# Optimization experiments

Measured on AMD Instinct MI355X. Metric: run time of the kernel, lower is better.

The kernel has to match this reference:

```python
import jax, jax.numpy as jnp
import numpy as np

B, S, D, H = 8192, 45, 64, 8
HD = D // H          # head_dim = 8
FF = 4 * D           # FFN inner dim = 256


def _layernorm(x, g, b, eps=1e-5):
    m = x.mean(-1, keepdims=True)
    v = ((x - m) ** 2).mean(-1, keepdims=True)
    return (x - m) * jax.lax.rsqrt(v + eps) * g + b


def setup_inputs() -> dict:
    key = jax.random.key(0)
    ks = jax.random.split(key, 8)
    s = 1.0 / np.sqrt(D)
    sf = 1.0 / np.sqrt(FF)
    return {
        "x": jax.random.normal(ks[0], (B, S, D), jnp.float32),
        "Wq": jax.random.normal(ks[1], (D, D), jnp.float32) * s,
        "bq": jnp.zeros((D,), jnp.float32),
        "Wk": jax.random.normal(ks[2], (D, D), jnp.float32) * s,
        "bk": jnp.zeros((D,), jnp.float32),
        "Wv": jax.random.normal(ks[3], (D, D), jnp.float32) * s,
        "bv": jnp.zeros((D,), jnp.float32),
        "Wo": jax.random.normal(ks[4], (D, D), jnp.float32) * s,
        "bo": jnp.zeros((D,), jnp.float32),
        "ln1_g": jnp.ones((D,), jnp.float32),
        "ln1_b": jnp.zeros((D,), jnp.float32),
        "W1": jax.random.normal(ks[5], (D, FF), jnp.float32) * s,
        "b1": jnp.zeros((FF,), jnp.float32),
        "W2": jax.random.normal(ks[6], (FF, D), jnp.float32) * sf,
        "b2": jnp.zeros((D,), jnp.float32),
        "ln2_g": jnp.ones((D,), jnp.float32),
        "ln2_b": jnp.zeros((D,), jnp.float32),
    }


def reference(x, Wq, bq, Wk, bk, Wv, bv, Wo, bo, ln1_g, ln1_b, W1, b1, W2, b2, ln2_g, ln2_b):
    b, s, d = x.shape
    # sinusoidal positional encoding (PositionalEncoding(hidden_dim, max_len=45))
    pos = jnp.arange(s, dtype=jnp.float32)[:, None]
    div = jnp.exp(-jnp.log(jnp.float32(10000.0)) * jnp.arange(0, d, 2, dtype=jnp.float32) / d)
    ang = pos * div                              # [S, D/2]
    pe = jnp.zeros((s, d), x.dtype).at[:, 0::2].set(jnp.sin(ang)).at[:, 1::2].set(jnp.cos(ang))
    h = x + pe                                   # [B, S, D]
    residual = h
    # torch.nn.MultiheadAttention, batch_first=True, 8 heads, head_dim 8
    q = (h @ Wq + bq).reshape(b, s, H, HD).transpose(0, 2, 1, 3)  # [B,H,S,HD]
    k = (h @ Wk + bk).reshape(b, s, H, HD).transpose(0, 2, 1, 3)
    v = (h @ Wv + bv).reshape(b, s, H, HD).transpose(0, 2, 1, 3)
    scores = jnp.einsum('bhqd,bhkd->bhqk', q, k) / jnp.sqrt(jnp.float32(HD))
    attn = jax.nn.softmax(scores, axis=-1)
    o = jnp.einsum('bhqk,bhkd->bhqd', attn, v).transpose(0, 2, 1, 3).reshape(b, s, d)
    o = o @ Wo + bo
    # norm(out + alpha * residual), alpha = 1
    h2 = _layernorm(o + residual, ln1_g, ln1_b)
    # FFN: Linear -> ReLU -> Linear, residual + LayerNorm (standard transformer FFN)
    f = jax.nn.relu(h2 @ W1 + b1) @ W2 + b2
    return _layernorm(h2 + f, ln2_g, ln2_b)
```

## Files before the change

kernel.cpp:

```cpp
#include <hip/hip_runtime.h>
#include <math.h>

#define NB 8192
#define S_ 45
#define D_ 64
#define FF_ 256
#define LDH 68
#define HBS 72
#define VTS 56
#define FBH 136

typedef __attribute__((ext_vector_type(4))) float f32x4;
typedef __attribute__((ext_vector_type(8))) short s16x8;
typedef __attribute__((ext_vector_type(4))) short s16x4;

#define WS_QKV 11520
#define WS_WO  36096
#define WS_W1  44288
#define WS_W2  77056

__device__ inline short f2bf(float f) {
    union { float f; unsigned u; } c; c.f = f;
    unsigned u = c.u;
    return (short)((u + 0x7FFFu + ((u >> 16) & 1u)) >> 16);
}
__device__ inline float bf2f(short s) {
    union { unsigned u; float f; } c;
    c.u = ((unsigned)(unsigned short)s) << 16;
    return c.f;
}

__global__ void prep_kernel(const float* __restrict__ Wq, const float* __restrict__ Wk,
                            const float* __restrict__ Wv, const float* __restrict__ Wo,
                            const float* __restrict__ W1, const float* __restrict__ W2,
                            void* __restrict__ ws) {
    float* pe   = (float*)ws;
    short* wqkv = (short*)((char*)ws + WS_QKV);
    short* wo   = (short*)((char*)ws + WS_WO);
    short* w1   = (short*)((char*)ws + WS_W1);
    short* w2   = (short*)((char*)ws + WS_W2);
    int i = blockIdx.x * 256 + threadIdx.x;
    if (i < S_ * D_) {
        int s = i / D_, d = i % D_;
        float div = expf(-logf(10000.0f) * (float)(d & ~1) / (float)D_);
        float ang = (float)s * div;
        pe[i] = (d & 1) ? cosf(ang) : sinf(ang);
    }
    if (i < 12288) {
        int n = i >> 6, k = i & 63;
        const float* W = (n < 64) ? Wq : (n < 128 ? Wk : Wv);
        wqkv[i] = f2bf(W[k * 64 + (n & 63)]);
    }
    if (i < 4096) {
        int n = i >> 6, k = i & 63;
        wo[i] = f2bf(Wo[k * 64 + n]);
    }
    if (i < 16384) {
        int n = i >> 6, k = i & 63;
        w1[i] = f2bf(W1[k * FF_ + n]);
        int n2 = i >> 8, k2 = i & 255;
        w2[i] = f2bf(W2[k2 * 64 + n2]);
    }
}

__launch_bounds__(512, 1)
__global__ void encoder_kernel(
    const float* __restrict__ x,
    const float* __restrict__ bq, const float* __restrict__ bk,
    const float* __restrict__ bv, const float* __restrict__ bo,
    const float* __restrict__ ln1g, const float* __restrict__ ln1b,
    const float* __restrict__ b1, const float* __restrict__ b2,
    const float* __restrict__ ln2g, const float* __restrict__ ln2b,
    const void* __restrict__ ws,
    float* __restrict__ out)
{
    const float* pe    = (const float*)ws;
    const short* wqkvT = (const short*)((const char*)ws + WS_QKV);
    const short* woT   = (const short*)((const char*)ws + WS_WO);
    const short* w1T   = (const short*)((const char*)ws + WS_W1);
    const short* w2T   = (const short*)((const char*)ws + WS_W2);

    __shared__ __align__(16) char pool[28800];
    short* hb = (short*)pool;
    short* qb = (short*)(pool + 6912);
    short* kb = (short*)(pool + 13824);
    short* vT = (short*)(pool + 20736);
    short* ob = qb;
    float* t1 = (float*)(pool + 13824);
    short* fb = (short*)(pool + 13824);
    float* t2 = (float*)(pool + 13824);

    const int t = threadIdx.x;
    const int b = blockIdx.x;
    const int w = t >> 6, l = t & 63;
    const int lr = l & 15, lg = l >> 4;
    const s16x8 zero8 = {0, 0, 0, 0, 0, 0, 0, 0};

    {
        const float4* x4 = (const float4*)(x + (size_t)b * (S_ * D_));
        const float4* p4 = (const float4*)pe;
        for (int i = t; i < S_ * D_ / 4; i += 512) {
            int r = i >> 4, c4 = (i & 15) << 2;
            float4 a = x4[i], p = p4[i];
            s16x4 hv16 = { f2bf(a.x + p.x), f2bf(a.y + p.y),
                           f2bf(a.z + p.z), f2bf(a.w + p.w) };
            *(s16x4*)&hb[r * HBS + c4] = hv16;
        }
        for (int i = t; i < 3 * HBS; i += 512) hb[45 * HBS + i] = 0;
    }
    __syncthreads();

    {
        const float SC2 = 0.35355339059327373f * 1.44269504088896340f;
        for (int id = w; id < 36; id += 8) {
            const int m0 = (id % 3) << 4, n0 = (id / 3) << 4;
            f32x4 acc = {0.f, 0.f, 0.f, 0.f};
            #pragma unroll
            for (int k0 = 0; k0 < 64; k0 += 32) {
                s16x8 af = *(const s16x8*)&hb[(m0 + lr) * HBS + k0 + lg * 8];
                s16x8 bf = *(const s16x8*)&wqkvT[(n0 + lr) * 64 + k0 + lg * 8];
                acc = __builtin_amdgcn_mfma_f32_16x16x32_bf16(af, bf, acc, 0, 0, 0);
            }
            if (n0 < 64) {
                const float bias = bq[n0 + lr];
                #pragma unroll
                for (int r = 0; r < 4; ++r)
                    qb[(m0 + lg * 4 + r) * HBS + n0 + lr] = f2bf((acc[r] + bias) * SC2);
            } else if (n0 < 128) {
                const int cc = n0 - 64 + lr;
                const float bias = bk[cc];
                #pragma unroll
                for (int r = 0; r < 4; ++r)
                    kb[(m0 + lg * 4 + r) * HBS + cc] = f2bf(acc[r] + bias);
            } else {
                const int cc = n0 - 128 + lr;
                const float bias = bv[cc];
                s16x4 vv = { f2bf(acc[0] + bias), f2bf(acc[1] + bias),
                             f2bf(acc[2] + bias), f2bf(acc[3] + bias) };
                *(s16x4*)&vT[cc * VTS + m0 + lg * 4] = vv;
            }
        }
    }
    __syncthreads();

    {
        const int hd = w << 3;
        s16x8 pv_b0 = *(const s16x8*)&vT[(hd + lr) * VTS + lg * 8];
        s16x8 pv_b1 = (lg < 2) ? *(const s16x8*)&vT[(hd + lr) * VTS + 32 + lg * 8]
                               : zero8;
        f32x4 O[3];
        #pragma unroll
        for (int tn = 0; tn < 3; ++tn) {
            s16x8 qbf = (lg == 0) ? *(const s16x8*)&qb[(tn * 16 + lr) * HBS + hd] : zero8;
            f32x4 S[3];
            #pragma unroll
            for (int tm = 0; tm < 3; ++tm) {
                s16x8 kaf = (lg == 0) ? *(const s16x8*)&kb[(tm * 16 + lr) * HBS + hd] : zero8;
                f32x4 z = {0.f, 0.f, 0.f, 0.f};
                S[tm] = __builtin_amdgcn_mfma_f32_16x16x32_bf16(kaf, qbf, z, 0, 0, 0);
            }
            float psum = 0.f;
            #pragma unroll
            for (int tm = 0; tm < 3; ++tm) {
                #pragma unroll
                for (int r = 0; r < 4; ++r) {
                    float e = __builtin_amdgcn_exp2f(S[tm][r]);
                    if (tm == 2) e = (lg * 4 + r >= 13) ? 0.f : e;
                    S[tm][r] = e;
                    psum += e;
                }
            }
            float s = psum;
            s += __shfl_xor(s, 16);
            s += __shfl_xor(s, 32);
            float inv = 1.0f / s;
            unsigned pk0[3], pk1[3];
            #pragma unroll
            for (int tm = 0; tm < 3; ++tm) {
                float a0 = S[tm][0] * inv, a1 = S[tm][1] * inv;
                float a2 = S[tm][2] * inv, a3 = S[tm][3] * inv;
                pk0[tm] = (__float_as_uint(a0) >> 16) | (__float_as_uint(a1) & 0xFFFF0000u);
                pk1[tm] = (__float_as_uint(a2) >> 16) | (__float_as_uint(a3) & 0xFFFF0000u);
            }
            const int srcA = lr + ((lg & 1) << 5);
            const int srcB = srcA + 16;
            unsigned gA0[3], gA1[3], gB0[3], gB1[3];
            #pragma unroll
            for (int tm = 0; tm < 3; ++tm) {
                gA0[tm] = (unsigned)__shfl((int)pk0[tm], srcA);
                gA1[tm] = (unsigned)__shfl((int)pk1[tm], srcA);
                gB0[tm] = (unsigned)__shfl((int)pk0[tm], srcB);
                gB1[tm] = (unsigned)__shfl((int)pk1[tm], srcB);
            }
            const bool tm1 = (lg >> 1) != 0;
            union { unsigned u[4]; s16x8 v; } a1c, a2c;
            a1c.u[0] = tm1 ? gA0[1] : gA0[0];
            a1c.u[1] = tm1 ? gA1[1] : gA1[0];
            a1c.u[2] = tm1 ? gB0[1] : gB0[0];
            a1c.u[3] = tm1 ? gB1[1] : gB1[0];
            const bool lo = (lg < 2);
            a2c.u[0] = lo ? gA0[2] : 0u;
            a2c.u[1] = lo ? gA1[2] : 0u;
            a2c.u[2] = lo ? gB0[2] : 0u;
            a2c.u[3] = lo ? gB1[2] : 0u;
            f32x4 z = {0.f, 0.f, 0.f, 0.f};
            O[tn] = __builtin_amdgcn_mfma_f32_16x16x32_bf16(a1c.v, pv_b0, z, 0, 0, 0);
            O[tn] = __builtin_amdgcn_mfma_f32_16x16x32_bf16(a2c.v, pv_b1, O[tn], 0, 0, 0);
        }
        __syncthreads();
        if (lr < 8) {
            #pragma unroll
            for (int tn = 0; tn < 3; ++tn)
                #pragma unroll
                for (int r = 0; r < 4; ++r) {
                    int row = tn * 16 + lg * 4 + r;
                    if (row < S_) ob[row * HBS + hd + lr] = f2bf(O[tn][r]);
                }
        }
    }
    __syncthreads();

    {
        for (int id = w; id < 12; id += 8) {
            const int m0 = (id % 3) << 4, n0 = (id / 3) << 4;
            f32x4 acc = {0.f, 0.f, 0.f, 0.f};
            #pragma unroll
            for (int k0 = 0; k0 < 64; k0 += 32) {
                s16x8 af = *(const s16x8*)&ob[(m0 + lr) * HBS + k0 + lg * 8];
                s16x8 bf = *(const s16x8*)&woT[(n0 + lr) * 64 + k0 + lg * 8];
                acc = __builtin_amdgcn_mfma_f32_16x16x32_bf16(af, bf, acc, 0, 0, 0);
            }
            const int col = n0 + lr;
            const float bias = bo[col];
            #pragma unroll
            for (int r = 0; r < 4; ++r) {
                int row = m0 + lg * 4 + r;
                if (row < S_)
                    t1[row * LDH + col] = acc[r] + bias + bf2f(hb[row * HBS + col]);
            }
        }
    }
    __syncthreads();

    {
        const int wv = t >> 6, d = t & 63;
        const float g = ln1g[d], bb = ln1b[d];
        for (int i = 0; i < 6; ++i) {
            int r = wv + 8 * i;
            if (r < S_) {
                float v = t1[r * LDH + d];
                float s = v, s2 = v * v;
                #pragma unroll
                for (int off = 32; off; off >>= 1) {
                    s  += __shfl_xor(s, off);
                    s2 += __shfl_xor(s2, off);
                }
                float mean = s * (1.0f / 64.0f);
                float var  = s2 * (1.0f / 64.0f) - mean * mean;
                float nv = (v - mean) * rsqrtf(var + 1e-5f);
                hb[r * HBS + d] = f2bf(nv * g + bb);
            }
        }
    }
    __syncthreads();

    f32x4 facc0 = {0.f, 0.f, 0.f, 0.f};
    f32x4 facc1 = {0.f, 0.f, 0.f, 0.f};
    for (int hx = 0; hx < 2; ++hx) {
        for (int id = w; id < 24; id += 8) {
            const int m0 = (id % 3) << 4, nl = (id / 3) << 4;
            f32x4 acc = {0.f, 0.f, 0.f, 0.f};
            #pragma unroll
            for (int k0 = 0; k0 < 64; k0 += 32) {
                s16x8 af = *(const s16x8*)&hb[(m0 + lr) * HBS + k0 + lg * 8];
                s16x8 bf = *(const s16x8*)&w1T[(hx * 128 + nl + lr) * 64 + k0 + lg * 8];
                acc = __builtin_amdgcn_mfma_f32_16x16x32_bf16(af, bf, acc, 0, 0, 0);
            }
            const float bias = b1[hx * 128 + nl + lr];
            #pragma unroll
            for (int r = 0; r < 4; ++r) {
                int row = m0 + lg * 4 + r;
                if (row < S_)
                    fb[row * FBH + nl + lr] = f2bf(fmaxf(acc[r] + bias, 0.f));
            }
        }
        __syncthreads();
        {
            const int m0 = (w % 3) << 4, n0 = (w / 3) << 4;
            #pragma unroll
            for (int k0 = 0; k0 < 128; k0 += 32) {
                s16x8 af = *(const s16x8*)&fb[(m0 + lr) * FBH + k0 + lg * 8];
                s16x8 bf = *(const s16x8*)&w2T[(n0 + lr) * 256 + hx * 128 + k0 + lg * 8];
                facc0 = __builtin_amdgcn_mfma_f32_16x16x32_bf16(af, bf, facc0, 0, 0, 0);
            }
        }
        if (w < 4) {
            const int id = w + 8;
            const int m0 = (id % 3) << 4, n0 = (id / 3) << 4;
            #pragma unroll
            for (int k0 = 0; k0 < 128; k0 += 32) {
                s16x8 af = *(const s16x8*)&fb[(m0 + lr) * FBH + k0 + lg * 8];
                s16x8 bf = *(const s16x8*)&w2T[(n0 + lr) * 256 + hx * 128 + k0 + lg * 8];
                facc1 = __builtin_amdgcn_mfma_f32_16x16x32_bf16(af, bf, facc1, 0, 0, 0);
            }
        }
        __syncthreads();
    }
    {
        const int m0 = (w % 3) << 4, n0 = (w / 3) << 4;
        const int col = n0 + lr;
        const float bias = b2[col];
        #pragma unroll
        for (int r = 0; r < 4; ++r) {
            int row = m0 + lg * 4 + r;
            if (row < S_)
                t2[row * LDH + col] = facc0[r] + bias + bf2f(hb[row * HBS + col]);
        }
        if (w < 4) {
            const int id = w + 8;
            const int m1 = (id % 3) << 4, n1 = (id / 3) << 4;
            const int col1 = n1 + lr;
            const float bias1 = b2[col1];
            #pragma unroll
            for (int r = 0; r < 4; ++r) {
                int row = m1 + lg * 4 + r;
                if (row < S_)
                    t2[row * LDH + col1] = facc1[r] + bias1 + bf2f(hb[row * HBS + col1]);
            }
        }
    }
    __syncthreads();

    {
        const int wv = t >> 6, d = t & 63;
        const float g = ln2g[d], bb = ln2b[d];
        for (int i = 0; i < 6; ++i) {
            int r = wv + 8 * i;
            if (r < S_) {
                float v = t2[r * LDH + d];
                float s = v, s2 = v * v;
                #pragma unroll
                for (int off = 32; off; off >>= 1) {
                    s  += __shfl_xor(s, off);
                    s2 += __shfl_xor(s2, off);
                }
                float mean = s * (1.0f / 64.0f);
                float var  = s2 * (1.0f / 64.0f) - mean * mean;
                float nv = (v - mean) * rsqrtf(var + 1e-5f);
                out[(size_t)b * (S_ * D_) + r * 64 + d] = nv * g + bb;
            }
        }
    }
}

extern "C" void kernel_launch(void* const* d_in, const int* in_sizes, int n_in,
                              void* d_out, int out_size, void* d_ws, size_t ws_size,
                              hipStream_t stream) {
    const float* x    = (const float*)d_in[0];
    const float* Wq   = (const float*)d_in[1];
    const float* bq   = (const float*)d_in[2];
    const float* Wk   = (const float*)d_in[3];
    const float* bk   = (const float*)d_in[4];
    const float* Wv   = (const float*)d_in[5];
    const float* bv   = (const float*)d_in[6];
    const float* Wo   = (const float*)d_in[7];
    const float* bo   = (const float*)d_in[8];
    const float* ln1g = (const float*)d_in[9];
    const float* ln1b = (const float*)d_in[10];
    const float* W1   = (const float*)d_in[11];
    const float* b1   = (const float*)d_in[12];
    const float* W2   = (const float*)d_in[13];
    const float* b2   = (const float*)d_in[14];
    const float* ln2g = (const float*)d_in[15];
    const float* ln2b = (const float*)d_in[16];
    float* out = (float*)d_out;

    hipLaunchKernelGGL(prep_kernel, dim3(64), dim3(256), 0, stream,
                       Wq, Wk, Wv, Wo, W1, W2, d_ws);
    hipLaunchKernelGGL(encoder_kernel, dim3(NB), dim3(512), 0, stream,
                       x, bq, bk, bv, bo, ln1g, ln1b, b1, b2, ln2g, ln2b,
                       d_ws, out);
}
```

Before: 321.5 us.

## Enlarge LDS pool to drop barriers in attention output and FFN halves

Grows the shared-memory pool so the attention output buffer gets its own region. Each wave can then write its P·V result to it directly without a barrier, instead of keeping three accumulators and syncing first. The FFN hidden layer is now computed at its full width of 256 into a wider LDS buffer, replacing two half passes. That removes two barriers per block and lets the second FFN matmul loop over the full K dimension. The cost is more LDS per block (about 38 KB) and a larger first FFN loop with 6 tiles per wave.

```diff
diff --git a/kernel.cpp b/kernel.cpp
--- a/kernel.cpp
+++ b/kernel.cpp
@@ -7,8 +7,8 @@
 #define FF_ 256
 #define LDH 68
 #define HBS 72
-#define VTS 56
-#define FBH 136
+#define VTS 72
+#define FBS 280
 
 typedef __attribute__((ext_vector_type(4))) float f32x4;
 typedef __attribute__((ext_vector_type(8))) short s16x8;
@@ -80,15 +80,15 @@
     const short* w1T   = (const short*)((const char*)ws + WS_W1);
     const short* w2T   = (const short*)((const char*)ws + WS_W2);
 
-    __shared__ __align__(16) char pool[28800];
+    __shared__ __align__(16) char pool[38016];
     short* hb = (short*)pool;
     short* qb = (short*)(pool + 6912);
     short* kb = (short*)(pool + 13824);
     short* vT = (short*)(pool + 20736);
-    short* ob = qb;
-    float* t1 = (float*)(pool + 13824);
-    short* fb = (short*)(pool + 13824);
-    float* t2 = (float*)(pool + 13824);
+    short* ob = (short*)(pool + 31104);
+    float* t1 = (float*)(pool + 6912);
+    short* fb = (short*)(pool + 6912);
+    float* t2 = (float*)(pool + 6912);
 
     const int t = threadIdx.x;
     const int b = blockIdx.x;
@@ -148,7 +148,6 @@
         s16x8 pv_b0 = *(const s16x8*)&vT[(hd + lr) * VTS + lg * 8];
         s16x8 pv_b1 = (lg < 2) ? *(const s16x8*)&vT[(hd + lr) * VTS + 32 + lg * 8]
                                : zero8;
-        f32x4 O[3];
         #pragma unroll
         for (int tn = 0; tn < 3; ++tn) {
             s16x8 qbf = (lg == 0) ? *(const s16x8*)&qb[(tn * 16 + lr) * HBS + hd] : zero8;
@@ -204,18 +203,15 @@
             a2c.u[2] = lo ? gB0[2] : 0u;
             a2c.u[3] = lo ? gB1[2] : 0u;
             f32x4 z = {0.f, 0.f, 0.f, 0.f};
-            O[tn] = __builtin_amdgcn_mfma_f32_16x16x32_bf16(a1c.v, pv_b0, z, 0, 0, 0);
-            O[tn] = __builtin_amdgcn_mfma_f32_16x16x32_bf16(a2c.v, pv_b1, O[tn], 0, 0, 0);
-        }
-        __syncthreads();
-        if (lr < 8) {
-            #pragma unroll
-            for (int tn = 0; tn < 3; ++tn)
+            f32x4 O = __builtin_amdgcn_mfma_f32_16x16x32_bf16(a1c.v, pv_b0, z, 0, 0, 0);
+            O = __builtin_amdgcn_mfma_f32_16x16x32_bf16(a2c.v, pv_b1, O, 0, 0, 0);
+            if (lr < 8) {
                 #pragma unroll
                 for (int r = 0; r < 4; ++r) {
                     int row = tn * 16 + lg * 4 + r;
-                    if (row < S_) ob[row * HBS + hd + lr] = f2bf(O[tn][r]);
+                    if (row < S_) ob[row * HBS + hd + lr] = f2bf(O[r]);
                 }
+            }
         }
     }
     __syncthreads();
@@ -264,48 +260,49 @@
     }
     __syncthreads();
 
-    f32x4 facc0 = {0.f, 0.f, 0.f, 0.f};
-    f32x4 facc1 = {0.f, 0.f, 0.f, 0.f};
-    for (int hx = 0; hx < 2; ++hx) {
-        for (int id = w; id < 24; id += 8) {
+    {
+        for (int id = w; id < 48; id += 8) {
             const int m0 = (id % 3) << 4, nl = (id / 3) << 4;
             f32x4 acc = {0.f, 0.f, 0.f, 0.f};
             #pragma unroll
             for (int k0 = 0; k0 < 64; k0 += 32) {
                 s16x8 af = *(const s16x8*)&hb[(m0 + lr) * HBS + k0 + lg * 8];
-                s16x8 bf = *(const s16x8*)&w1T[(hx * 128 + nl + lr) * 64 + k0 + lg * 8];
+                s16x8 bf = *(const s16x8*)&w1T[(nl + lr) * 64 + k0 + lg * 8];
                 acc = __builtin_amdgcn_mfma_f32_16x16x32_bf16(af, bf, acc, 0, 0, 0);
             }
-            const float bias = b1[hx * 128 + nl + lr];
+            const float bias = b1[nl + lr];
             #pragma unroll
             for (int r = 0; r < 4; ++r) {
                 int row = m0 + lg * 4 + r;
                 if (row < S_)
-                    fb[row * FBH + nl + lr] = f2bf(fmaxf(acc[r] + bias, 0.f));
-            }
-        }
-        __syncthreads();
-        {
-            const int m0 = (w % 3) << 4, n0 = (w / 3) << 4;
-            #pragma unroll
-            for (int k0 = 0; k0 < 128; k0 += 32) {
-                s16x8 af = *(const s16x8*)&fb[(m0 + lr) * FBH + k0 + lg * 8];
-                s16x8 bf = *(const s16x8*)&w2T[(n0 + lr) * 256 + hx * 128 + k0 + lg * 8];
-                facc0 = __builtin_amdgcn_mfma_f32_16x16x32_bf16(af, bf, facc0, 0, 0, 0);
-            }
+                    fb[row * FBS + nl + lr] = f2bf(fmaxf(acc[r] + bias, 0.f));
+            }
+        }
+    }
+    __syncthreads();
+
+    f32x4 facc0 = {0.f, 0.f, 0.f, 0.f};
+    f32x4 facc1 = {0.f, 0.f, 0.f, 0.f};
+    {
+        const int m0 = (w % 3) << 4, n0 = (w / 3) << 4;
+        #pragma unroll 4
+        for (int k0 = 0; k0 < FF_; k0 += 32) {
+            s16x8 af = *(const s16x8*)&fb[(m0 + lr) * FBS + k0 + lg * 8];
+            s16x8 bf = *(const s16x8*)&w2T[(n0 + lr) * 256 + k0 + lg * 8];
+            facc0 = __builtin_amdgcn_mfma_f32_16x16x32_bf16(af, bf, facc0, 0, 0, 0);
         }
         if (w < 4) {
             const int id = w + 8;
-            const int m0 = (id % 3) << 4, n0 = (id / 3) << 4;
-            #pragma unroll
-            for (int k0 = 0; k0 < 128; k0 += 32) {
-                s16x8 af = *(const s16x8*)&fb[(m0 + lr) * FBH + k0 + lg * 8];
-                s16x8 bf = *(const s16x8*)&w2T[(n0 + lr) * 256 + hx * 128 + k0 + lg * 8];
+            const int m1 = (id % 3) << 4, n1 = (id / 3) << 4;
+            #pragma unroll 4
+            for (int k0 = 0; k0 < FF_; k0 += 32) {
+                s16x8 af = *(const s16x8*)&fb[(m1 + lr) * FBS + k0 + lg * 8];
+                s16x8 bf = *(const s16x8*)&w2T[(n1 + lr) * 256 + k0 + lg * 8];
                 facc1 = __builtin_amdgcn_mfma_f32_16x16x32_bf16(af, bf, facc1, 0, 0, 0);
             }
         }
-        __syncthreads();
-    }
+    }
+    __syncthreads();
     {
         const int m0 = (w % 3) << 4, n0 = (w / 3) << 4;
         const int col = n0 + lr;
```

Measured after the change: 325.0 us. About the same (+1.1%).
